# Kernel optimization log

Measured on AMD Instinct MI355X. Metric: run time of the kernel, lower is better.

## Reference

```python
import jax, jax.numpy as jnp
import numpy as np

D_IN = 1024
D_OUT = 1024
NUM_HEADS = 16
HEAD_DIM = D_OUT // NUM_HEADS


def setup_inputs() -> dict:
    key = jax.random.key(0)
    ks = jax.random.split(key, 6)
    B, S = 2, 2048
    scale = 1.0 / np.sqrt(D_IN)
    x = jax.random.normal(ks[0], (B, S, D_IN), dtype=jnp.float32)
    # Linear weights stored torch-style as [out_features, in_features]
    Wq = jax.random.normal(ks[1], (D_OUT, D_IN), dtype=jnp.float32) * scale
    Wk = jax.random.normal(ks[2], (D_OUT, D_IN), dtype=jnp.float32) * scale
    Wv = jax.random.normal(ks[3], (D_OUT, D_IN), dtype=jnp.float32) * scale
    Wo = jax.random.normal(ks[4], (D_OUT, D_IN), dtype=jnp.float32) * scale
    bo = jax.random.normal(ks[5], (D_OUT,), dtype=jnp.float32) * 0.01
    return {"x": x, "Wq": Wq, "Wk": Wk, "Wv": Wv, "Wo": Wo, "bo": bo}


def reference(x, Wq, Wk, Wv, Wo, bo):
    B, S, _ = x.shape
    H, hd = NUM_HEADS, HEAD_DIM
    # QKV projections (qkv_bias=False), split into heads: [B, H, S, hd]
    q = (x @ Wq.T).reshape(B, S, H, hd).transpose(0, 2, 1, 3)
    k = (x @ Wk.T).reshape(B, S, H, hd).transpose(0, 2, 1, 3)
    v = (x @ Wv.T).reshape(B, S, H, hd).transpose(0, 2, 1, 3)
    # scaled causal attention scores [B, H, S, S]
    scores = jnp.einsum("bhqd,bhkd->bhqk", q, k) / jnp.sqrt(jnp.float32(hd))
    causal = jnp.tril(jnp.ones((S, S), dtype=bool))
    scores = jnp.where(causal, scores, jnp.finfo(scores.dtype).min)
    attn = jax.nn.softmax(scores, axis=-1)  # dropout p=0.0 -> identity
    ctx = jnp.einsum("bhqk,bhkd->bhqd", attn, v)  # [B, H, S, hd]
    ctx = ctx.transpose(0, 2, 1, 3).reshape(B, S, H * hd)
    return ctx @ Wo.T + bo
```

## Files before the change

kernel.cpp:

```cpp
#include <hip/hip_runtime.h>
#include <hip/hip_bf16.h>

#define AS1 __attribute__((address_space(1)))
#define AS3 __attribute__((address_space(3)))

typedef __attribute__((ext_vector_type(4))) float floatx4;
typedef __attribute__((ext_vector_type(8))) short bf16x8;
typedef unsigned short u16;
typedef unsigned int u32;

__device__ __forceinline__ u16 f2b(float f) {
  u32 u = __builtin_bit_cast(u32, f);
  u += 0x7fffu + ((u >> 16) & 1u);
  return (u16)(u >> 16);
}
__device__ __forceinline__ u32 pk2(float lo, float hi) {
  __hip_bfloat162 h = __float22bfloat162_rn(float2{lo, hi});
  u32 u;
  __builtin_memcpy(&u, &h, 4);
  return u;
}
__device__ __forceinline__ bf16x8 cvt8(float4 a, float4 b) {
  uint4 u{pk2(a.x, a.y), pk2(a.z, a.w), pk2(b.x, b.y), pk2(b.z, b.w)};
  return __builtin_bit_cast(bf16x8, u);
}

__device__ __forceinline__ void gld16(const void* g, AS3 u32* l) {
  __builtin_amdgcn_global_load_lds((const AS1 u32*)(const AS1 void*)g, l, 16,
                                   0, 0);
}

#define QSCALE 0.18033688011112042f
#define QSHIFT 14.4269504088896f

__global__ __launch_bounds__(256) void cvt_all(
    const float* __restrict__ x, const float* __restrict__ wq,
    const float* __restrict__ wk, const float* __restrict__ wv,
    const float* __restrict__ wo, u16* __restrict__ xb, u16* __restrict__ wqb,
    u16* __restrict__ wkb, u16* __restrict__ wvb, u16* __restrict__ wob) {
  const int i = blockIdx.x * 256 + threadIdx.x;
  const float* src;
  u16* dst;
  int off;
  if (i < 524288) {
    src = x; dst = xb; off = i;
  } else {
    const int j = i - 524288;
    const int wsel = j >> 17;
    off = j & 131071;
    src = (wsel == 0) ? wq : (wsel == 1) ? wk : (wsel == 2) ? wv : wo;
    dst = (wsel == 0) ? wqb : (wsel == 1) ? wkb : (wsel == 2) ? wvb : wob;
  }
  const float4* p = (const float4*)(src + (size_t)off * 8);
  *(bf16x8*)(dst + (size_t)off * 8) = cvt8(p[0], p[1]);
}

__device__ __forceinline__ void gemm_bf16(const u16* __restrict__ A,
                                          const u16* __restrict__ B, short* sA,
                                          short* sB, floatx4 acc[4][4]) {
  const int tid = threadIdx.x;
  const int lane = tid & 63;
  const int w = tid >> 6;
  const int l15 = lane & 15, quad = lane >> 4;
  const int wm = w >> 1, wn = w & 1;

  const u16* ga = A + ((size_t)(w * 32 + (lane >> 2))) * 1024 + (lane & 3) * 8;
  const u16* gb = B + ((size_t)(w * 32 + (lane >> 2))) * 1024 + (lane & 3) * 8;
  AS3 u32* la = (AS3 u32*)(AS3 short*)sA + w * 512;
  AS3 u32* lb = (AS3 u32*)(AS3 short*)sB + w * 512;

  for (int kt = 0; kt < 32; ++kt) {
    __syncthreads();
    gld16(ga, la);
    gld16(ga + (size_t)16 * 1024, la + 256);
    gld16(gb, lb);
    gld16(gb + (size_t)16 * 1024, lb + 256);
    ga += 32;
    gb += 32;
    __syncthreads();

    bf16x8 af[4], bfr[4];
#pragma unroll
    for (int mc = 0; mc < 4; ++mc)
      af[mc] = *(const bf16x8*)&sA[(wm * 64 + mc * 16 + l15) * 32 + quad * 8];
#pragma unroll
    for (int nc = 0; nc < 4; ++nc)
      bfr[nc] = *(const bf16x8*)&sB[(wn * 64 + nc * 16 + l15) * 32 + quad * 8];
#pragma unroll
    for (int mc = 0; mc < 4; ++mc)
#pragma unroll
      for (int nc = 0; nc < 4; ++nc)
        acc[mc][nc] = __builtin_amdgcn_mfma_f32_16x16x32_bf16(
            af[mc], bfr[nc], acc[mc][nc], 0, 0, 0);
  }
}

__device__ __forceinline__ void qkv_epilogue(floatx4 acc[4][4], int m0, int nb,
                                             int sel, u16* __restrict__ Q,
                                             u16* __restrict__ K,
                                             u16* __restrict__ Vt) {
  const int tid = threadIdx.x;
  const int lane = tid & 63, w = tid >> 6;
  const int l15 = lane & 15, quad = lane >> 4;
  const int wm = w >> 1, wn = w & 1;
#pragma unroll
  for (int mc = 0; mc < 4; ++mc) {
#pragma unroll
    for (int nc = 0; nc < 4; ++nc) {
      const int nn = nb + wn * 64 + nc * 16 + l15;
      const int h = nn >> 6, d = nn & 63;
#pragma unroll
      for (int r = 0; r < 4; ++r) {
        const int m = m0 + wm * 64 + mc * 16 + quad * 4 + r;
        const int b = m >> 11, s = m & 2047;
        const int bh = b * 16 + h;
        float av = acc[mc][nc][r];
        if (sel == 0) av *= QSCALE;
        const u16 v = f2b(av);
        if (sel == 0)
          Q[((size_t)bh * 2048 + s) * 64 + d] = v;
        else if (sel == 1)
          K[((size_t)bh * 2048 + s) * 64 + d] = v;
        else
          Vt[((size_t)bh * 64 + d) * 2048 + s] = v;
      }
    }
  }
}

__global__ __launch_bounds__(256) void qkv_gemm_b(
    const u16* __restrict__ xb, const u16* __restrict__ Wqb,
    const u16* __restrict__ Wkb, const u16* __restrict__ Wvb,
    u16* __restrict__ Q, u16* __restrict__ K, u16* __restrict__ Vt) {
  __shared__ __align__(16) short smem[2 * 128 * 32];
  const int m0 = blockIdx.x * 128;
  const int by = blockIdx.y;
  const int sel = by >> 3;
  const int nb = (by & 7) * 128;
  const u16* W = (sel == 0) ? Wqb : (sel == 1) ? Wkb : Wvb;

  floatx4 acc[4][4];
#pragma unroll
  for (int i = 0; i < 4; i++)
#pragma unroll
    for (int j = 0; j < 4; j++) acc[i][j] = (floatx4)0.0f;
  gemm_bf16(xb + (size_t)m0 * 1024, W + (size_t)nb * 1024, smem,
            smem + 128 * 32, acc);
  qkv_epilogue(acc, m0, nb, sel, Q, K, Vt);
}

__global__ __launch_bounds__(256) void out_gemm_b(const u16* __restrict__ ctx,
                                                  const u16* __restrict__ Wob,
                                                  const float* __restrict__ bo,
                                                  float* __restrict__ out) {
  __shared__ __align__(16) short smem[128 * 32 + 64 * 32];
  const int tid = threadIdx.x;
  const int lane = tid & 63, w = tid >> 6;
  const int l15 = lane & 15, quad = lane >> 4;
  const int m0 = blockIdx.x * 128;
  const int n0 = blockIdx.y * 64;
  short* sA = smem;
  short* sB = smem + 128 * 32;

  const u16* ga = ctx + ((size_t)(m0 + w * 32 + (lane >> 2))) * 1024 +
                  (lane & 3) * 8;
  const u16* gb = Wob + ((size_t)(n0 + w * 16 + (lane >> 2))) * 1024 +
                  (lane & 3) * 8;
  AS3 u32* la = (AS3 u32*)(AS3 short*)sA + w * 512;
  AS3 u32* lb = (AS3 u32*)(AS3 short*)sB + w * 256;

  floatx4 acc[2][4];
#pragma unroll
  for (int i = 0; i < 2; i++)
#pragma unroll
    for (int j = 0; j < 4; j++) acc[i][j] = (floatx4)0.0f;

  for (int kt = 0; kt < 32; ++kt) {
    __syncthreads();
    gld16(ga, la);
    gld16(ga + (size_t)16 * 1024, la + 256);
    gld16(gb, lb);
    ga += 32;
    gb += 32;
    __syncthreads();

    bf16x8 af[2], bfr[4];
#pragma unroll
    for (int mc = 0; mc < 2; ++mc)
      af[mc] = *(const bf16x8*)&sA[(w * 32 + mc * 16 + l15) * 32 + quad * 8];
#pragma unroll
    for (int nc = 0; nc < 4; ++nc)
      bfr[nc] = *(const bf16x8*)&sB[(nc * 16 + l15) * 32 + quad * 8];
#pragma unroll
    for (int mc = 0; mc < 2; ++mc)
#pragma unroll
      for (int nc = 0; nc < 4; ++nc)
        acc[mc][nc] = __builtin_amdgcn_mfma_f32_16x16x32_bf16(
            af[mc], bfr[nc], acc[mc][nc], 0, 0, 0);
  }

#pragma unroll
  for (int mc = 0; mc < 2; ++mc)
#pragma unroll
    for (int nc = 0; nc < 4; ++nc) {
      const int n = n0 + nc * 16 + l15;
      const float bias = bo[n];
#pragma unroll
      for (int r = 0; r < 4; ++r) {
        const int m = m0 + w * 32 + mc * 16 + quad * 4 + r;
        out[(size_t)m * 1024 + n] = acc[mc][nc][r] + bias;
      }
    }
}

template <bool F32A>
__device__ __forceinline__ void gemm128(const void* __restrict__ A,
                                        const float* __restrict__ B, short* sA,
                                        short* sB, floatx4 acc[4][4]) {
  const int tid = threadIdx.x;
  const int lane = tid & 63;
  const int w = tid >> 6;
  const int l15 = lane & 15, quad = lane >> 4;
  const int wm = w >> 1, wn = w & 1;
  const int srow = tid >> 1;
  const int scb = (tid & 1) * 16;

  float4 pa[4], pb[4];
  int4 pa16[2];
  if constexpr (F32A) {
    const float* ap = (const float*)A + (size_t)srow * 1024 + scb;
    pa[0] = ((const float4*)ap)[0]; pa[1] = ((const float4*)ap)[1];
    pa[2] = ((const float4*)ap)[2]; pa[3] = ((const float4*)ap)[3];
  } else {
    const u16* ap = (const u16*)A + (size_t)srow * 1024 + scb;
    pa16[0] = ((const int4*)ap)[0]; pa16[1] = ((const int4*)ap)[1];
  }
  {
    const float* bp = B + (size_t)srow * 1024 + scb;
    pb[0] = ((const float4*)bp)[0]; pb[1] = ((const float4*)bp)[1];
    pb[2] = ((const float4*)bp)[2]; pb[3] = ((const float4*)bp)[3];
  }

  for (int kt = 0; kt < 32; ++kt) {
    __syncthreads();
    if constexpr (F32A) {
      *(bf16x8*)&sA[srow * 40 + scb] = cvt8(pa[0], pa[1]);
      *(bf16x8*)&sA[srow * 40 + scb + 8] = cvt8(pa[2], pa[3]);
    } else {
      *(int4*)&sA[srow * 40 + scb] = pa16[0];
      *(int4*)&sA[srow * 40 + scb + 8] = pa16[1];
    }
    *(bf16x8*)&sB[srow * 40 + scb] = cvt8(pb[0], pb[1]);
    *(bf16x8*)&sB[srow * 40 + scb + 8] = cvt8(pb[2], pb[3]);
    __syncthreads();

    if (kt < 31) {
      const int k0 = (kt + 1) * 32;
      if constexpr (F32A) {
        const float* ap = (const float*)A + (size_t)srow * 1024 + k0 + scb;
        pa[0] = ((const float4*)ap)[0]; pa[1] = ((const float4*)ap)[1];
        pa[2] = ((const float4*)ap)[2]; pa[3] = ((const float4*)ap)[3];
      } else {
        const u16* ap = (const u16*)A + (size_t)srow * 1024 + k0 + scb;
        pa16[0] = ((const int4*)ap)[0]; pa16[1] = ((const int4*)ap)[1];
      }
      const float* bp = B + (size_t)srow * 1024 + k0 + scb;
      pb[0] = ((const float4*)bp)[0]; pb[1] = ((const float4*)bp)[1];
      pb[2] = ((const float4*)bp)[2]; pb[3] = ((const float4*)bp)[3];
    }

    bf16x8 af[4], bfr[4];
#pragma unroll
    for (int mc = 0; mc < 4; ++mc)
      af[mc] = *(const bf16x8*)&sA[(wm * 64 + mc * 16 + l15) * 40 + quad * 8];
#pragma unroll
    for (int nc = 0; nc < 4; ++nc)
      bfr[nc] = *(const bf16x8*)&sB[(wn * 64 + nc * 16 + l15) * 40 + quad * 8];
#pragma unroll
    for (int mc = 0; mc < 4; ++mc)
#pragma unroll
      for (int nc = 0; nc < 4; ++nc)
        acc[mc][nc] = __builtin_amdgcn_mfma_f32_16x16x32_bf16(
            af[mc], bfr[nc], acc[mc][nc], 0, 0, 0);
  }
}

__global__ __launch_bounds__(256) void qkv_gemm_f(
    const float* __restrict__ x, const float* __restrict__ Wq,
    const float* __restrict__ Wk, const float* __restrict__ Wv,
    u16* __restrict__ Q, u16* __restrict__ K, u16* __restrict__ Vt) {
  __shared__ __align__(16) short smem[2 * 128 * 40];
  const int m0 = blockIdx.x * 128;
  const int by = blockIdx.y;
  const int sel = by >> 3;
  const int nb = (by & 7) * 128;
  const float* W = (sel == 0) ? Wq : (sel == 1) ? Wk : Wv;

  floatx4 acc[4][4];
#pragma unroll
  for (int i = 0; i < 4; i++)
#pragma unroll
    for (int j = 0; j < 4; j++) acc[i][j] = (floatx4)0.0f;
  gemm128<true>((const void*)(x + (size_t)m0 * 1024), W + (size_t)nb * 1024,
                smem, smem + 128 * 40, acc);
  qkv_epilogue(acc, m0, nb, sel, Q, K, Vt);
}

__global__ __launch_bounds__(256) void out_gemm_f(const u16* __restrict__ ctx,
                                                  const float* __restrict__ Wo,
                                                  const float* __restrict__ bo,
                                                  float* __restrict__ out) {
  __shared__ __align__(16) short smem[2 * 128 * 40];
  const int tid = threadIdx.x;
  const int lane = tid & 63, w = tid >> 6;
  const int l15 = lane & 15, quad = lane >> 4;
  const int wm = w >> 1, wn = w & 1;
  const int m0 = blockIdx.x * 128;
  const int n0 = blockIdx.y * 128;

  floatx4 acc[4][4];
#pragma unroll
  for (int i = 0; i < 4; i++)
#pragma unroll
    for (int j = 0; j < 4; j++) acc[i][j] = (floatx4)0.0f;
  gemm128<false>((const void*)(ctx + (size_t)m0 * 1024),
                 Wo + (size_t)n0 * 1024, smem, smem + 128 * 40, acc);

#pragma unroll
  for (int mc = 0; mc < 4; ++mc)
#pragma unroll
    for (int nc = 0; nc < 4; ++nc) {
      const int n = n0 + wn * 64 + nc * 16 + l15;
      const float bias = bo[n];
#pragma unroll
      for (int r = 0; r < 4; ++r) {
        const int m = m0 + wm * 64 + mc * 16 + quad * 4 + r;
        out[(size_t)m * 1024 + n] = acc[mc][nc][r] + bias;
      }
    }
}

template <bool CLEAN>
__device__ __forceinline__ void attn_tile(const u16* __restrict__ sKb,
                                          const u16* __restrict__ sVb,
                                          const int l15, const int quad,
                                          const int jbase, const int wrow,
                                          const bf16x8 aQ0, const bf16x8 aQ1,
                                          floatx4 (&acc)[4], floatx4& lsv) {
  if constexpr (CLEAN) {
    bf16x8 ka[2][4];
    uint2 va[2][8];
#pragma unroll
    for (int u = 0; u < 4; ++u) {
      const u16* kp0 = sKb + l15 * 72 + quad * 8;
      ka[0][u] = *(const bf16x8*)(kp0 + (u >> 1) * (16 * 72) + (u & 1) * 32);
    }
#pragma unroll
    for (int dt = 0; dt < 4; ++dt) {
      const u16* vp = sVb + (dt * 16 + l15) * 136 + quad * 4;
      va[0][2 * dt] = *(const uint2*)(vp);
      va[0][2 * dt + 1] = *(const uint2*)(vp + 16);
    }
#pragma unroll
    for (int kp = 0; kp < 4; ++kp) {
      const int pc = kp & 1, pn = (kp + 1) & 1;
      if (kp < 3) {
        const u16* kp1 = sKb + ((kp + 1) * 32 + l15) * 72 + quad * 8;
#pragma unroll
        for (int u = 0; u < 4; ++u)
          ka[pn][u] =
              *(const bf16x8*)(kp1 + (u >> 1) * (16 * 72) + (u & 1) * 32);
#pragma unroll
        for (int dt = 0; dt < 4; ++dt) {
          const u16* vp =
              sVb + (dt * 16 + l15) * 136 + (kp + 1) * 32 + quad * 4;
          va[pn][2 * dt] = *(const uint2*)(vp);
          va[pn][2 * dt + 1] = *(const uint2*)(vp + 16);
        }
      }
      floatx4 st0 = (floatx4)0.0f, st1 = (floatx4)0.0f;
      __builtin_amdgcn_s_setprio(1);
      st0 = __builtin_amdgcn_mfma_f32_16x16x32_bf16(ka[pc][0], aQ0, st0, 0, 0,
                                                    0);
      st1 = __builtin_amdgcn_mfma_f32_16x16x32_bf16(ka[pc][2], aQ0, st1, 0, 0,
                                                    0);
      st0 = __builtin_amdgcn_mfma_f32_16x16x32_bf16(ka[pc][1], aQ1, st0, 0, 0,
                                                    0);
      st1 = __builtin_amdgcn_mfma_f32_16x16x32_bf16(ka[pc][3], aQ1, st1, 0, 0,
                                                    0);
      __builtin_amdgcn_s_setprio(0);
      float p0[4], p1[4];
#pragma unroll
      for (int r = 0; r < 4; ++r) {
        p0[r] = __builtin_amdgcn_exp2f(st0[r] - QSHIFT);
        p1[r] = __builtin_amdgcn_exp2f(st1[r] - QSHIFT);
      }
#pragma unroll
      for (int r = 0; r < 4; ++r) lsv[r] += p0[r] + p1[r];
      uint4 pfu{pk2(p0[0], p0[1]), pk2(p0[2], p0[3]), pk2(p1[0], p1[1]),
                pk2(p1[2], p1[3])};
      const bf16x8 pf8 = __builtin_bit_cast(bf16x8, pfu);
      __builtin_amdgcn_s_setprio(1);
#pragma unroll
      for (int dt = 0; dt < 4; ++dt) {
        uint4 avu{va[pc][2 * dt].x, va[pc][2 * dt].y, va[pc][2 * dt + 1].x,
                  va[pc][2 * dt + 1].y};
        bf16x8 av8 = __builtin_bit_cast(bf16x8, avu);
        acc[dt] = __builtin_amdgcn_mfma_f32_16x16x32_bf16(av8, pf8, acc[dt],
                                                          0, 0, 0);
      }
      __builtin_amdgcn_s_setprio(0);
    }
  } else {
#pragma unroll 2
    for (int kp = 0; kp < 4; ++kp) {
      const int kbase = jbase + kp * 32;
      if (kbase > wrow + 15) break;

      const u16* kr0 = sKb + (kp * 32 + l15) * 72 + quad * 8;
      bf16x8 ak00 = *(const bf16x8*)(kr0);
      bf16x8 ak01 = *(const bf16x8*)(kr0 + 32);
      floatx4 st0 = (floatx4)0.0f;
      st0 = __builtin_amdgcn_mfma_f32_16x16x32_bf16(ak00, aQ0, st0, 0, 0, 0);
      st0 = __builtin_amdgcn_mfma_f32_16x16x32_bf16(ak01, aQ1, st0, 0, 0, 0);

      const bool have1 = (kbase + 16 <= wrow + 15);
      floatx4 st1 = (floatx4)0.0f;
      if (have1) {
        const u16* kr1 = kr0 + 16 * 72;
        bf16x8 ak10 = *(const bf16x8*)(kr1);
        bf16x8 ak11 = *(const bf16x8*)(kr1 + 32);
        st1 = __builtin_amdgcn_mfma_f32_16x16x32_bf16(ak10, aQ0, st1, 0, 0, 0);
        st1 = __builtin_amdgcn_mfma_f32_16x16x32_bf16(ak11, aQ1, st1, 0, 0, 0);
      }

      float p0[4], p1[4];
      const bool m0b = (kbase + 15 > wrow);
#pragma unroll
      for (int r = 0; r < 4; ++r) {
        float t = st0[r] - QSHIFT;
        if (m0b && (kbase + quad * 4 + r > wrow + l15)) t = -1e30f;
        p0[r] = __builtin_amdgcn_exp2f(t);
      }
      if (have1) {
        const bool m1b = (kbase + 31 > wrow);
#pragma unroll
        for (int r = 0; r < 4; ++r) {
          float t = st1[r] - QSHIFT;
          if (m1b && (kbase + 16 + quad * 4 + r > wrow + l15)) t = -1e30f;
          p1[r] = __builtin_amdgcn_exp2f(t);
        }
      } else {
        p1[0] = p1[1] = p1[2] = p1[3] = 0.0f;
      }
#pragma unroll
      for (int r = 0; r < 4; ++r) lsv[r] += p0[r] + p1[r];

      uint4 pfu{pk2(p0[0], p0[1]), pk2(p0[2], p0[3]), pk2(p1[0], p1[1]),
                pk2(p1[2], p1[3])};
      const bf16x8 pf8 = __builtin_bit_cast(bf16x8, pfu);

#pragma unroll
      for (int dt = 0; dt < 4; ++dt) {
        const u16* vp = sVb + (dt * 16 + l15) * 136 + kp * 32 + quad * 4;
        uint2 v0 = *(const uint2*)(vp);
        uint2 v1 = *(const uint2*)(vp + 16);
        uint4 avu{v0.x, v0.y, v1.x, v1.y};
        bf16x8 av8 = __builtin_bit_cast(bf16x8, avu);
        acc[dt] = __builtin_amdgcn_mfma_f32_16x16x32_bf16(av8, pf8, acc[dt],
                                                          0, 0, 0);
      }
    }
  }
}

__device__ __forceinline__ void attn_write(u16* tw, const floatx4 (&acc)[4],
                                           const floatx4 lsv, const int l15,
                                           const int quad, const int wrow,
                                           const int b, const int h,
                                           u16* __restrict__ ctx) {
  float lsum = (lsv[0] + lsv[1]) + (lsv[2] + lsv[3]);
  lsum += __shfl_xor(lsum, 16, 64);
  lsum += __shfl_xor(lsum, 32, 64);
  const float inv = 1.0f / lsum;
#pragma unroll
  for (int dt = 0; dt < 4; ++dt) {
    uint2 o2{pk2(acc[dt][0] * inv, acc[dt][1] * inv),
             pk2(acc[dt][2] * inv, acc[dt][3] * inv)};
    *(uint2*)&tw[l15 * 72 + dt * 16 + quad * 4] = o2;
  }
  bf16x8 o0 = *(const bf16x8*)&tw[l15 * 72 + quad * 16];
  bf16x8 o1 = *(const bf16x8*)&tw[l15 * 72 + quad * 16 + 8];
  u16* cp =
      ctx + ((size_t)(b * 2048 + wrow + l15)) * 1024 + h * 64 + quad * 16;
  *(bf16x8*)cp = o0;
  *(bf16x8*)(cp + 8) = o1;
}

__global__ __launch_bounds__(512, 2) void attn_kernel(
    const u16* __restrict__ Q, const u16* __restrict__ K,
    const u16* __restrict__ Vt, u16* __restrict__ ctx) {
  const int bid = blockIdx.x;
  const int pr = bid >> 5;
  const int bh = bid & 31;
  const int tid = threadIdx.x;
  const int w = tid >> 6;
  const int lane = tid & 63;
  const int l15 = lane & 15;
  const int quad = lane >> 4;

  constexpr int KE = 128 * 72;
  constexpr int VE = 64 * 136;
  constexpr int BUF = KE + VE;
  __shared__ __align__(16) u16 lds[2 * BUF];

  const int kr = tid >> 2, kc = (tid & 3) * 16;
  const int vd = tid >> 3, vc = (tid & 7) * 16;
  const int b = bh >> 4, h = bh & 15;

  const u16* Kg = K + (size_t)bh * 2048 * 64;
  const u16* Vg = Vt + (size_t)bh * 64 * 2048;

  const int cA = 15 - pr, cB = pr;
  const int wrowA = cA * 128 + w * 16;
  const int wrowB = cB * 128 + w * 16;

  bf16x8 aQA0, aQA1, aQB0, aQB1;
  {
    const u16* qa = Q + ((size_t)bh * 2048 + wrowA + l15) * 64 + quad * 8;
    aQA0 = *(const bf16x8*)(qa);
    aQA1 = *(const bf16x8*)(qa + 32);
    const u16* qb = Q + ((size_t)bh * 2048 + wrowB + l15) * 64 + quad * 8;
    aQB0 = *(const bf16x8*)(qb);
    aQB1 = *(const bf16x8*)(qb + 32);
  }

  floatx4 accA[4], accB[4];
#pragma unroll
  for (int i = 0; i < 4; ++i) {
    accA[i] = (floatx4)0.0f;
    accB[i] = (floatx4)0.0f;
  }
  floatx4 lsvA = (floatx4)0.0f, lsvB = (floatx4)0.0f;

  int4 pk[2], pv[2];
  pk[0] = *(const int4*)(Kg + (size_t)kr * 64 + kc);
  pk[1] = *(const int4*)(Kg + (size_t)kr * 64 + kc + 8);
  pv[0] = *(const int4*)(Vg + (size_t)vd * 2048 + vc);
  pv[1] = *(const int4*)(Vg + (size_t)vd * 2048 + vc + 8);
  *(int4*)&lds[kr * 72 + kc] = pk[0];
  *(int4*)&lds[kr * 72 + kc + 8] = pk[1];
  *(int4*)&lds[KE + vd * 136 + vc] = pv[0];
  *(int4*)&lds[KE + vd * 136 + vc + 8] = pv[1];
  __syncthreads();
  int cur = 0;

  for (int jb = 0; jb <= cA; ++jb) {
    const u16* sKb = lds + cur * BUF;
    const u16* sVb = sKb + KE;

    const int jn = (jb < cA) ? (jb + 1) * 128 : -1;
    if (jn >= 0) {
      pk[0] = *(const int4*)(Kg + (size_t)(jn + kr) * 64 + kc);
      pk[1] = *(const int4*)(Kg + (size_t)(jn + kr) * 64 + kc + 8);
      pv[0] = *(const int4*)(Vg + (size_t)vd * 2048 + jn + vc);
      pv[1] = *(const int4*)(Vg + (size_t)vd * 2048 + jn + vc + 8);
    }

    const int jbase = jb * 128;
    if (jb < cA)
      attn_tile<true>(sKb, sVb, l15, quad, jbase, wrowA, aQA0, aQA1, accA,
                      lsvA);
    else
      attn_tile<false>(sKb, sVb, l15, quad, jbase, wrowA, aQA0, aQA1, accA,
                       lsvA);
    if (jb < cB)
      attn_tile<true>(sKb, sVb, l15, quad, jbase, wrowB, aQB0, aQB1, accB,
                      lsvB);
    else if (jb == cB)
      attn_tile<false>(sKb, sVb, l15, quad, jbase, wrowB, aQB0, aQB1, accB,
                       lsvB);

    if (jn >= 0) {
      u16* dK = lds + (cur ^ 1) * BUF;
      u16* dV = dK + KE;
      *(int4*)&dK[kr * 72 + kc] = pk[0];
      *(int4*)&dK[kr * 72 + kc + 8] = pk[1];
      *(int4*)&dV[vd * 136 + vc] = pv[0];
      *(int4*)&dV[vd * 136 + vc + 8] = pv[1];
    }
    __syncthreads();
    cur ^= 1;
  }

  u16* tw = lds + (cur ^ 1) * BUF + (w * 16) * 72;
  attn_write(tw, accA, lsvA, l15, quad, wrowA, b, h, ctx);
  attn_write(tw, accB, lsvB, l15, quad, wrowB, b, h, ctx);
}

extern "C" void kernel_launch(void* const* d_in, const int* in_sizes, int n_in,
                              void* d_out, int out_size, void* d_ws,
                              size_t ws_size, hipStream_t stream) {
  const float* x = (const float*)d_in[0];
  const float* Wq = (const float*)d_in[1];
  const float* Wk = (const float*)d_in[2];
  const float* Wv = (const float*)d_in[3];
  const float* Wo = (const float*)d_in[4];
  const float* bo = (const float*)d_in[5];
  float* out = (float*)d_out;

  u16* Q = (u16*)d_ws;
  u16* K = Q + (size_t)4096 * 1024;
  u16* Vt = K + (size_t)4096 * 1024;
  u16* ctx = Vt + (size_t)4096 * 1024;

  if (ws_size >= (size_t)40 * 1024 * 1024) {
    u16* xb = ctx;
    u16* Wqb = (u16*)d_ws + (size_t)16 * 1024 * 1024;
    u16* Wkb = Wqb + (size_t)1024 * 1024;
    u16* Wvb = Wkb + (size_t)1024 * 1024;
    u16* Wob = Wvb + (size_t)1024 * 1024;

    cvt_all<<<4096, 256, 0, stream>>>(x, Wq, Wk, Wv, Wo, xb, Wqb, Wkb, Wvb,
                                      Wob);
    qkv_gemm_b<<<dim3(32, 24), 256, 0, stream>>>(xb, Wqb, Wkb, Wvb, Q, K, Vt);
    attn_kernel<<<256, 512, 0, stream>>>(Q, K, Vt, ctx);
    out_gemm_b<<<dim3(32, 16), 256, 0, stream>>>(ctx, Wob, bo, out);
  } else {
    qkv_gemm_f<<<dim3(32, 24), 256, 0, stream>>>(x, Wq, Wk, Wv, Q, K, Vt);
    attn_kernel<<<256, 512, 0, stream>>>(Q, K, Vt, ctx);
    out_gemm_f<<<dim3(32, 8), 256, 0, stream>>>(ctx, Wo, bo, out);
  }
}
```

Baseline: 194.9 us.

## Split paired causal query tiles into separate blocks with longest-first ordering

The attention kernel used to pair query tile 15-p with tile p in one block, so every block did equal causal work but K/V tiles were shared across two query tiles. It now launches 512 blocks, each owning one 128-row query tile, and orders them so the longest tiles (c=15..8) are scheduled first and the short ones fill in afterwards. Launch bounds are raised to 4 blocks per CU to allow higher occupancy. This doubles K/V global loads and LDS staging per query row and relies on the hardware scheduler for load balance instead of the static pairing.

```diff
diff --git a/kernel.cpp b/kernel.cpp
--- a/kernel.cpp
+++ b/kernel.cpp
@@ -497,12 +497,13 @@
   *(bf16x8*)(cp + 8) = o1;
 }
 
-__global__ __launch_bounds__(512, 2) void attn_kernel(
+__global__ __launch_bounds__(512, 4) void attn_kernel(
     const u16* __restrict__ Q, const u16* __restrict__ K,
     const u16* __restrict__ Vt, u16* __restrict__ ctx) {
   const int bid = blockIdx.x;
-  const int pr = bid >> 5;
+  const int s = bid >> 5;
   const int bh = bid & 31;
+  const int c = (s < 8) ? (15 - s) : (s - 8);
   const int tid = threadIdx.x;
   const int w = tid >> 6;
   const int lane = tid & 63;
@@ -521,27 +522,19 @@
   const u16* Kg = K + (size_t)bh * 2048 * 64;
   const u16* Vg = Vt + (size_t)bh * 64 * 2048;
 
-  const int cA = 15 - pr, cB = pr;
-  const int wrowA = cA * 128 + w * 16;
-  const int wrowB = cB * 128 + w * 16;
-
-  bf16x8 aQA0, aQA1, aQB0, aQB1;
+  const int wrow = c * 128 + w * 16;
+
+  bf16x8 aQ0, aQ1;
   {
-    const u16* qa = Q + ((size_t)bh * 2048 + wrowA + l15) * 64 + quad * 8;
-    aQA0 = *(const bf16x8*)(qa);
-    aQA1 = *(const bf16x8*)(qa + 32);
-    const u16* qb = Q + ((size_t)bh * 2048 + wrowB + l15) * 64 + quad * 8;
-    aQB0 = *(const bf16x8*)(qb);
-    aQB1 = *(const bf16x8*)(qb + 32);
-  }
-
-  floatx4 accA[4], accB[4];
-#pragma unroll
-  for (int i = 0; i < 4; ++i) {
-    accA[i] = (floatx4)0.0f;
-    accB[i] = (floatx4)0.0f;
-  }
-  floatx4 lsvA = (floatx4)0.0f, lsvB = (floatx4)0.0f;
+    const u16* qp = Q + ((size_t)bh * 2048 + wrow + l15) * 64 + quad * 8;
+    aQ0 = *(const bf16x8*)(qp);
+    aQ1 = *(const bf16x8*)(qp + 32);
+  }
+
+  floatx4 acc[4];
+#pragma unroll
+  for (int i = 0; i < 4; ++i) acc[i] = (floatx4)0.0f;
+  floatx4 lsv = (floatx4)0.0f;
 
   int4 pk[2], pv[2];
   pk[0] = *(const int4*)(Kg + (size_t)kr * 64 + kc);
@@ -555,11 +548,11 @@
   __syncthreads();
   int cur = 0;
 
-  for (int jb = 0; jb <= cA; ++jb) {
+  for (int jb = 0; jb <= c; ++jb) {
     const u16* sKb = lds + cur * BUF;
     const u16* sVb = sKb + KE;
 
-    const int jn = (jb < cA) ? (jb + 1) * 128 : -1;
+    const int jn = (jb < c) ? (jb + 1) * 128 : -1;
     if (jn >= 0) {
       pk[0] = *(const int4*)(Kg + (size_t)(jn + kr) * 64 + kc);
       pk[1] = *(const int4*)(Kg + (size_t)(jn + kr) * 64 + kc + 8);
@@ -568,18 +561,10 @@
     }
 
     const int jbase = jb * 128;
-    if (jb < cA)
-      attn_tile<true>(sKb, sVb, l15, quad, jbase, wrowA, aQA0, aQA1, accA,
-                      lsvA);
+    if (jb < c)
+      attn_tile<true>(sKb, sVb, l15, quad, jbase, wrow, aQ0, aQ1, acc, lsv);
     else
-      attn_tile<false>(sKb, sVb, l15, quad, jbase, wrowA, aQA0, aQA1, accA,
-                       lsvA);
-    if (jb < cB)
-      attn_tile<true>(sKb, sVb, l15, quad, jbase, wrowB, aQB0, aQB1, accB,
-                      lsvB);
-    else if (jb == cB)
-      attn_tile<false>(sKb, sVb, l15, quad, jbase, wrowB, aQB0, aQB1, accB,
-                       lsvB);
+      attn_tile<false>(sKb, sVb, l15, quad, jbase, wrow, aQ0, aQ1, acc, lsv);
 
     if (jn >= 0) {
       u16* dK = lds + (cur ^ 1) * BUF;
@@ -594,8 +579,7 @@
   }
 
   u16* tw = lds + (cur ^ 1) * BUF + (w * 16) * 72;
-  attn_write(tw, accA, lsvA, l15, quad, wrowA, b, h, ctx);
-  attn_write(tw, accB, lsvB, l15, quad, wrowB, b, h, ctx);
+  attn_write(tw, acc, lsv, l15, quad, wrow, b, h, ctx);
 }
 
 extern "C" void kernel_launch(void* const* d_in, const int* in_sizes, int n_in,
@@ -624,11 +608,11 @@
     cvt_all<<<4096, 256, 0, stream>>>(x, Wq, Wk, Wv, Wo, xb, Wqb, Wkb, Wvb,
                                       Wob);
     qkv_gemm_b<<<dim3(32, 24), 256, 0, stream>>>(xb, Wqb, Wkb, Wvb, Q, K, Vt);
-    attn_kernel<<<256, 512, 0, stream>>>(Q, K, Vt, ctx);
+    attn_kernel<<<512, 512, 0, stream>>>(Q, K, Vt, ctx);
     out_gemm_b<<<dim3(32, 16), 256, 0, stream>>>(ctx, Wob, bo, out);
   } else {
     qkv_gemm_f<<<dim3(32, 24), 256, 0, stream>>>(x, Wq, Wk, Wv, Q, K, Vt);
-    attn_kernel<<<256, 512, 0, stream>>>(Q, K, Vt, ctx);
+    attn_kernel<<<512, 512, 0, stream>>>(Q, K, Vt, ctx);
     out_gemm_f<<<dim3(32, 8), 256, 0, stream>>>(ctx, Wo, bo, out);
   }
 }
```

Result: no change. 198.4 us (+1.8%).
